# Optimization experiments

Measured on AMD Instinct MI355X. Metric: run time of the kernel, lower is better.

## Reference

```python
import jax, jax.numpy as jnp
import numpy as np

USER_NUM, ITEM_NUM = 50000, 25000
N_U, N_I = 4096, 4096
N_E, N_PRED = 262144, 65536
D, K, N_LAYERS = 64, 1000, 3
SSL_TEMP, SSL_REG, ALPHA, PROTO_REG = 0.1, 1e-6, 1.0, 8e-8


def setup_inputs() -> dict:
    key = jax.random.key(0)
    ks = jax.random.split(key, 16)
    return {
        "emb_user": jax.random.normal(ks[0], (USER_NUM, D), jnp.float32),
        "emb_item": jax.random.normal(ks[1], (ITEM_NUM, D), jnp.float32),
        "user_centroids": jax.random.normal(ks[2], (K, D), jnp.float32),
        "item_centroids": jax.random.normal(ks[3], (K, D), jnp.float32),
        "edge_u": jax.random.randint(ks[4], (N_E,), 0, N_U, jnp.int32),
        "edge_v": jax.random.randint(ks[5], (N_E,), 0, N_I, jnp.int32),
        "pos_u": jax.random.randint(ks[6], (N_PRED,), 0, N_U, jnp.int32),
        "pos_v": jax.random.randint(ks[7], (N_PRED,), 0, N_I, jnp.int32),
        "neg_u": jax.random.randint(ks[8], (N_PRED,), 0, N_U, jnp.int32),
        "neg_v": jax.random.randint(ks[9], (N_PRED,), 0, N_I, jnp.int32),
        "idx_user": jax.random.randint(ks[10], (N_U,), 0, USER_NUM, jnp.int32),
        "idx_item": jax.random.randint(ks[11], (N_I,), 0, ITEM_NUM, jnp.int32),
        "user2cluster": jax.random.randint(ks[12], (USER_NUM,), 0, K, jnp.int32),
        "item2cluster": jax.random.randint(ks[13], (ITEM_NUM,), 0, K, jnp.int32),
    }


def _l2norm(x, eps=1e-12):  # F.normalize(p=2, dim=1)
    return x / jnp.maximum(jnp.linalg.norm(x, axis=1, keepdims=True), eps)


def _ssl_loss(cur, prev, prev_total):
    nc, npv, nt = _l2norm(cur), _l2norm(prev), _l2norm(prev_total)
    pos = jnp.exp(jnp.sum(nc * npv, axis=1) / SSL_TEMP)            # [B]
    tot = jnp.exp(nc @ nt.T / SSL_TEMP).sum(axis=1)                 # [B]
    return -jnp.log(pos / tot).sum()


def _proto_loss(emb, idx, node2cluster, centroids):
    ne = _l2norm(emb)
    cents = _l2norm(centroids)                                      # run_kmeans normalizes centroids
    my_cent = cents[node2cluster[idx]]                              # [B, D]
    pos = jnp.exp(jnp.sum(ne * my_cent, axis=1) / SSL_TEMP)
    tot = jnp.exp(ne @ cents.T / SSL_TEMP).sum(axis=1)
    return -jnp.log(pos / tot).sum()


def reference(emb_user, emb_item, user_centroids, item_centroids,
              edge_u, edge_v, pos_u, pos_v, neg_u, neg_v,
              idx_user, idx_item, user2cluster, item2cluster):
    # --- symmetric-normalized bipartite GraphConv (norm='both', no weight/bias) ---
    ones_e = jnp.ones((N_E,), jnp.float32)
    deg_u = jax.ops.segment_sum(ones_e, edge_u, num_segments=N_U)
    deg_i = jax.ops.segment_sum(ones_e, edge_v, num_segments=N_I)
    inv_u = (1.0 / jnp.sqrt(jnp.maximum(deg_u, 1.0)))[:, None]      # [N_U,1]
    inv_i = (1.0 / jnp.sqrt(jnp.maximum(deg_i, 1.0)))[:, None]      # [N_I,1]

    e_u = emb_user[idx_user]                                        # initial subgraph embeddings
    e_i = emb_item[idx_item]
    res_u, res_i = e_u, e_i
    h_u, h_i = e_u, e_i
    for _ in range(N_LAYERS):
        m_u = (h_u * inv_u)[edge_u]                                 # messages along rate edges
        m_i = (h_i * inv_i)[edge_v]                                 # messages along rated-by edges
        new_i = jax.ops.segment_sum(m_u, edge_v, num_segments=N_I) * inv_i
        new_u = jax.ops.segment_sum(m_i, edge_u, num_segments=N_U) * inv_u
        h_u, h_i = new_u, new_i
        res_u = res_u + h_u
        res_i = res_i + h_i

    # --- structural-neighbour SSL loss (last layer output vs layer-0 embeddings) ---
    ssl_u = _ssl_loss(h_u, e_u, emb_user)
    ssl_i = _ssl_loss(h_i, e_i, emb_item)
    ssl_loss = SSL_REG * (ssl_u + ALPHA * ssl_i)

    # --- protoNCE loss (raw embedding-table rows vs kmeans centroids) ---
    proto_loss = PROTO_REG * (
        _proto_loss(emb_user[idx_user], idx_user, user2cluster, user_centroids)
        + _proto_loss(emb_item[idx_item], idx_item, item2cluster, item_centroids)
    )

    res_u = res_u / (N_LAYERS + 1)
    res_i = res_i / (N_LAYERS + 1)

    # --- HeteroDotProductPredictor: u_dot_v on 'rate' edges -> [E,1] ---
    pos_score = jnp.sum(res_u[pos_u] * res_i[pos_v], axis=1, keepdims=True)
    neg_score = jnp.sum(res_u[neg_u] * res_i[neg_v], axis=1, keepdims=True)
    return pos_score, neg_score, ssl_loss, proto_loss
```

## Files before the change

kernel.cpp:

```cpp
#include <hip/hip_runtime.h>
#include <hip/hip_bf16.h>

#define NU 4096
#define NI 4096
#define NE 262144
#define NPRED 65536
#define DD 64
#define KCL 1000
#define UNUM 50000
#define INUM 25000
#define INUM_PAD 25008
#define KCL_PAD 1008

typedef short sh8 __attribute__((ext_vector_type(8)));
typedef float f4 __attribute__((ext_vector_type(4)));

__device__ __forceinline__ float wred64(float x){
#pragma unroll
  for(int m=1;m<64;m<<=1) x += __shfl_xor(x,m);
  return x;
}

__device__ __forceinline__ float fast_exp2(float x){
  return __builtin_amdgcn_exp2f(x);
}

#define HB 1024
#define HN0 (HB+12500)
#define HN1 (HN0+6252)
#define HN2 (HN1+252)
#define HN3 (HN2+252)

__global__ void k_histnorm(const int* __restrict__ eu, const int* __restrict__ ev,
                           int* cu, int* ci,
                           const float* __restrict__ emb_u, const float* __restrict__ emb_i,
                           const float* __restrict__ ucent, const float* __restrict__ icent,
                           __hip_bfloat16* ntb_u, __hip_bfloat16* ntb_i,
                           __hip_bfloat16* ncb_u, __hip_bfloat16* ncb_i){
  int b = blockIdx.x;
  if(b < HB){
    int t = b*256 + threadIdx.x;
    atomicAdd(&cu[eu[t]],1); atomicAdd(&ci[ev[t]],1);
    return;
  }
  const float* in; __hip_bfloat16* outp; int rows; int base;
  if(b < HN0)      { in=emb_u; outp=ntb_u; rows=UNUM; base=HB; }
  else if(b < HN1) { in=emb_i; outp=ntb_i; rows=INUM; base=HN0; }
  else if(b < HN2) { in=ucent; outp=ncb_u; rows=KCL;  base=HN1; }
  else             { in=icent; outp=ncb_i; rows=KCL;  base=HN2; }
  int row = (b-base)*4 + (threadIdx.x>>6);
  int lane = threadIdx.x & 63;
  if(row >= rows){ outp[row*DD + lane] = __float2bfloat16(0.f); return; }
  float v = in[row*DD + lane];
  float s = wred64(v*v);
  float sc = 1.0f / fmaxf(sqrtf(s), 1e-12f);
  outp[row*DD + lane] = __float2bfloat16(v*sc);
}

__global__ void k_scan(const int* cnt_u, int* rp_u, int* cur_u, float* inv_u,
                       const int* cnt_i, int* rp_i, int* cur_i, float* inv_i,
                       float* tot4){
  {
    int base = blockIdx.x*8192 + threadIdx.x*8;
#pragma unroll
    for(int k=0;k<8;k++) tot4[base+k] = 0.f;
  }
  const int* cnt = blockIdx.x ? cnt_i : cnt_u;
  int* rp  = blockIdx.x ? rp_i  : rp_u;
  int* cur = blockIdx.x ? cur_i : cur_u;
  float* inv = blockIdx.x ? inv_i : inv_u;
  __shared__ int sdata[1024];
  int tid = threadIdx.x;
  int v[4]; int s = 0;
#pragma unroll
  for(int k=0;k<4;k++){ v[k]=cnt[tid*4+k]; s+=v[k]; }
  sdata[tid]=s; __syncthreads();
  for(int off=1; off<1024; off<<=1){
    int add = (tid>=off)? sdata[tid-off] : 0;
    __syncthreads();
    if(tid>=off) sdata[tid] += add;
    __syncthreads();
  }
  int run = sdata[tid]-s;
#pragma unroll
  for(int k=0;k<4;k++){
    int idx = tid*4+k;
    rp[idx]=run; cur[idx]=run;
    inv[idx] = 1.0f/sqrtf(fmaxf((float)v[k],1.0f));
    run += v[k];
  }
  if(tid==1023) rp[4096]=run;
}

__global__ void k_fillgather(const int* __restrict__ eu, const int* __restrict__ ev,
                             int* cur_u, int* cur_i, int* adj_u, int* adj_i,
                             const float* __restrict__ emb_u, const float* __restrict__ emb_i,
                             const int* __restrict__ idx_u, const int* __restrict__ idx_i,
                             const float* __restrict__ inv_u, const float* __restrict__ inv_i,
                             float* e_u, float* e_i, float* res_u, float* res_i,
                             float* hs_u, float* hs_i){
  int b = blockIdx.x;
  if(b < 1024){
    int t = b*256 + threadIdx.x;
    int u=eu[t], v=ev[t];
    adj_u[atomicAdd(&cur_u[u],1)] = v;
    adj_i[atomicAdd(&cur_i[v],1)] = u;
  } else {
    int t = (b-1024)*256 + threadIdx.x;
    const int half = NU*DD;
    if(t < half){
      int r=t>>6;
      float v = emb_u[idx_u[r]*DD + (t&63)];
      e_u[t]=v; res_u[t]=v; hs_u[t]=v*inv_u[r];
    } else {
      int s=t-half; int r=s>>6;
      float v = emb_i[idx_i[r]*DD + (s&63)];
      e_i[s]=v; res_i[s]=v; hs_i[s]=v*inv_i[r];
    }
  }
}

__global__ void k_conv(const int* __restrict__ rp_i, const int* __restrict__ adj_i,
                       const float* __restrict__ hsu_in, const float* __restrict__ inv_i,
                       float* h_i, float* res_i, float* hsi_out,
                       const int* __restrict__ rp_u, const int* __restrict__ adj_u,
                       const float* __restrict__ hsi_in, const float* __restrict__ inv_u,
                       float* h_u, float* res_u, float* hsu_out){
  int b = blockIdx.x*4 + (threadIdx.x>>6);
  int lane = threadIdx.x & 63;
  const int* rp; const int* adj; const float* srcv; const float* inv;
  float *h, *res, *hso; int node;
  if(b < NI){ rp=rp_i; adj=adj_i; srcv=hsu_in; inv=inv_i; h=h_i; res=res_i; hso=hsi_out; node=b; }
  else      { node=b-NI; rp=rp_u; adj=adj_u; srcv=hsi_in; inv=inv_u; h=h_u; res=res_u; hso=hsu_out; }
  int s=rp[node], e=rp[node+1];
  float acc=0.f;
  for(int base=s; base<e; base+=64){
    int m = e-base;
    int myidx = adj[base + min(lane, m-1)];
    int kk = min(64, m);
    int k=0;
    for(; k+8<=kk; k+=8){
      int i0=__shfl(myidx,k  ), i1=__shfl(myidx,k+1),
          i2=__shfl(myidx,k+2), i3=__shfl(myidx,k+3),
          i4=__shfl(myidx,k+4), i5=__shfl(myidx,k+5),
          i6=__shfl(myidx,k+6), i7=__shfl(myidx,k+7);
      float v0=srcv[i0*DD+lane], v1=srcv[i1*DD+lane],
            v2=srcv[i2*DD+lane], v3=srcv[i3*DD+lane],
            v4=srcv[i4*DD+lane], v5=srcv[i5*DD+lane],
            v6=srcv[i6*DD+lane], v7=srcv[i7*DD+lane];
      acc += ((v0+v1)+(v2+v3)) + ((v4+v5)+(v6+v7));
    }
    for(; k<kk; k++) acc += srcv[__shfl(myidx,k)*DD+lane];
  }
  float iv = inv[node];
  float outv = acc*iv;
  h[node*DD+lane] = outv;
  res[node*DD+lane] += outv;
  hso[node*DD+lane] = outv*iv;
}

#define PB0 1024
#define PB1 (PB0+1024)
#define PB2 (PB1+1024)
#define PB3 (PB2+1024)
#define PB4 (PB3+1024)

__global__ void k_normpos(const float* __restrict__ h_u, const float* __restrict__ h_i,
                          const float* __restrict__ e_u, const float* __restrict__ e_i,
                          const float* __restrict__ ucent, const float* __restrict__ icent,
                          __hip_bfloat16* nc_u, __hip_bfloat16* nc_i,
                          __hip_bfloat16* npv_u, __hip_bfloat16* npv_i,
                          const int* __restrict__ idx_u, const int* __restrict__ idx_i,
                          const int* __restrict__ u2c, const int* __restrict__ i2c,
                          float* pos4){
  const float SC = 14.426950408889634f;
  int b = blockIdx.x;
  int lane = threadIdx.x & 63;
  if(b >= PB3){
    int w = (b-PB3)*4 + (threadIdx.x>>6);
    float hu=h_u[w*DD+lane], eu=e_u[w*DD+lane];
    float hi=h_i[w*DD+lane], ei=e_i[w*DD+lane];
    int cu = u2c[idx_u[w]], ci = i2c[idx_i[w]];
    float cuv = ucent[cu*DD+lane], civ = icent[ci*DD+lane];
    float hh = wred64(hu*hu), ee = wred64(eu*eu), he = wred64(hu*eu);
    float h2 = wred64(hi*hi), e2 = wred64(ei*ei), hei= wred64(hi*ei);
    float ccu= wred64(cuv*cuv), ecu = wred64(eu*cuv);
    float cci= wred64(civ*civ), eci = wred64(ei*civ);
    if(lane==0){
      const float eps=1e-12f;
      pos4[0*NU+w] = he  / (fmaxf(sqrtf(hh),eps)*fmaxf(sqrtf(ee),eps));
      pos4[1*NU+w] = hei / (fmaxf(sqrtf(h2),eps)*fmaxf(sqrtf(e2),eps));
      pos4[2*NU+w] = ecu / (fmaxf(sqrtf(ee),eps)*fmaxf(sqrtf(ccu),eps));
      pos4[3*NU+w] = eci / (fmaxf(sqrtf(e2),eps)*fmaxf(sqrtf(cci),eps));
    }
    return;
  }
  const float* in; __hip_bfloat16* outp; int base;
  if(b < PB0)      { in=h_u; outp=nc_u;  base=0; }
  else if(b < PB1) { in=h_i; outp=nc_i;  base=PB0; }
  else if(b < PB2) { in=e_u; outp=npv_u; base=PB1; }
  else             { in=e_i; outp=npv_i; base=PB2; }
  int row = (b-base)*4 + (threadIdx.x>>6);
  float v = in[row*DD + lane];
  float s = wred64(v*v);
  float sc = SC / fmaxf(sqrtf(s), 1e-12f);
  outp[row*DD + lane] = __float2bfloat16(v*sc);
}

struct EArg {
  const __hip_bfloat16* A; const __hip_bfloat16* B; float* tot;
  int nBpad; int jchunk; int ny;
};
struct SArg {
  const float* res_u; const float* res_i;
  const int* pu; const int* pv; const int* nu; const int* nv; float* out;
};
#define EGX 784

__global__ __launch_bounds__(256,4)
void k_expsum(EArg e0, EArg e1, EArg e2, EArg e3, SArg sc){
  if(blockIdx.z == 4){
    const int stride = EGX*256;
    const int limit = 2*NPRED*16;
    for(int t = blockIdx.x*256 + threadIdx.x; t < limit; t += stride){
      int pair = t >> 4;
      int sl = t & 15;
      int a,b;
      if(pair < NPRED){ a=sc.pu[pair]; b=sc.pv[pair]; }
      else { a=sc.nu[pair-NPRED]; b=sc.nv[pair-NPRED]; }
      f4 xu = *(const f4*)(sc.res_u + a*DD + sl*4);
      f4 xv = *(const f4*)(sc.res_i + b*DD + sl*4);
      float x = xu[0]*xv[0] + xu[1]*xv[1] + xu[2]*xv[2] + xu[3]*xv[3];
      x += __shfl_xor(x,1); x += __shfl_xor(x,2);
      x += __shfl_xor(x,4); x += __shfl_xor(x,8);
      if(sl==0) sc.out[pair] = x*(1.0f/16.0f);
    }
    return;
  }
  EArg e = (blockIdx.z==0)? e0 : (blockIdx.z==1)? e1 : (blockIdx.z==2)? e2 : e3;
  int bid = blockIdx.x;
  int g = bid >> 6, r6 = bid & 63;
  int y = 8*g + (r6 & 7);
  int x = r6 >> 3;
  if(y >= e.ny) return;
  int wave = threadIdx.x >> 6;
  int lane = threadIdx.x & 63;
  int row0 = (x*4 + wave)*128;
  int j_begin = y*e.jchunk;
  int j_end = min(j_begin + e.jchunk, e.nBpad);
  int r = lane & 15, kq = (lane>>4)*8;

  sh8 a0[8], a1[8];
#pragma unroll
  for(int t=0;t<8;t++){
    const short* ap = (const short*)(e.A + (row0 + t*16 + r)*DD);
    a0[t] = *(const sh8*)(ap + kq);
    a1[t] = *(const sh8*)(ap + kq + 32);
  }
  float acc[8][4];
#pragma unroll
  for(int t=0;t<8;t++)
#pragma unroll
    for(int q=0;q<4;q++) acc[t][q]=0.f;

  const short* bbase = (const short*)e.B;
  const short* bp0 = bbase + (j_begin + r)*DD + kq;
  sh8 b0 = *(const sh8*)(bp0);
  sh8 b1 = *(const sh8*)(bp0 + 32);

#pragma unroll 2
  for(int j0=j_begin; j0<j_end; j0+=16){
    const short* np = bbase + (j0 + 16 + r)*DD + kq;
    sh8 n0 = *(const sh8*)(np);
    sh8 n1 = *(const sh8*)(np + 32);
#pragma unroll
    for(int t=0;t<8;t++){
      f4 c = {0.f,0.f,0.f,0.f};
      c = __builtin_amdgcn_mfma_f32_16x16x32_bf16(a0[t], b0, c, 0,0,0);
      c = __builtin_amdgcn_mfma_f32_16x16x32_bf16(a1[t], b1, c, 0,0,0);
#pragma unroll
      for(int q=0;q<4;q++) acc[t][q] += fast_exp2(c[q]);
    }
    b0 = n0; b1 = n1;
  }
#pragma unroll
  for(int t=0;t<8;t++){
#pragma unroll
    for(int q=0;q<4;q++){
      float v = acc[t][q];
      v += __shfl_xor(v,1); v += __shfl_xor(v,2);
      v += __shfl_xor(v,4); v += __shfl_xor(v,8);
      if(r==0) atomicAdd(&e.tot[row0 + t*16 + (lane>>4)*4 + q], v);
    }
  }
}

__global__ void k_loss(const float* __restrict__ tot4, const float* __restrict__ pos4,
                       float* out){
  const float PI_ = (float)(INUM_PAD-INUM);
  const float PK_ = (float)(KCL_PAD-KCL);
  float s0=0,s1=0,s2=0,s3=0;
  for(int b=threadIdx.x; b<NU; b+=256){
    s0 += logf(tot4[0*NU+b])       - 10.f*pos4[0*NU+b];
    s1 += logf(tot4[1*NU+b] - PI_) - 10.f*pos4[1*NU+b];
    s2 += logf(tot4[2*NU+b] - PK_) - 10.f*pos4[2*NU+b];
    s3 += logf(tot4[3*NU+b] - PK_) - 10.f*pos4[3*NU+b];
  }
  s0=wred64(s0); s1=wred64(s1); s2=wred64(s2); s3=wred64(s3);
  __shared__ float ls[4][4];
  int lane=threadIdx.x&63, w=threadIdx.x>>6;
  if(lane==0){ ls[w][0]=s0; ls[w][1]=s1; ls[w][2]=s2; ls[w][3]=s3; }
  __syncthreads();
  if(threadIdx.x==0){
    float a=0,b2=0,c=0,d=0;
#pragma unroll
    for(int k=0;k<4;k++){ a+=ls[k][0]; b2+=ls[k][1]; c+=ls[k][2]; d+=ls[k][3]; }
    out[2*NPRED]   = 1e-6f*(a+b2);
    out[2*NPRED+1] = 8e-8f*(c+d);
  }
}

extern "C" void kernel_launch(void* const* d_in, const int* in_sizes, int n_in,
                              void* d_out, int out_size, void* d_ws, size_t ws_size,
                              hipStream_t stream) {
  const float* emb_user = (const float*)d_in[0];
  const float* emb_item = (const float*)d_in[1];
  const float* ucent    = (const float*)d_in[2];
  const float* icent    = (const float*)d_in[3];
  const int* edge_u = (const int*)d_in[4];
  const int* edge_v = (const int*)d_in[5];
  const int* pos_u  = (const int*)d_in[6];
  const int* pos_v  = (const int*)d_in[7];
  const int* neg_u  = (const int*)d_in[8];
  const int* neg_v  = (const int*)d_in[9];
  const int* idx_u  = (const int*)d_in[10];
  const int* idx_i  = (const int*)d_in[11];
  const int* u2c    = (const int*)d_in[12];
  const int* i2c    = (const int*)d_in[13];
  float* out = (float*)d_out;

  char* w = (char*)d_ws;
  auto alloc = [&](size_t bytes)->void*{
    void* p = (void*)w;
    w += (bytes + 255) & ~(size_t)255;
    return p;
  };
  int* cnt_u = (int*)alloc(NU*4);
  int* cnt_i = (int*)alloc(NI*4);
  int* rp_u  = (int*)alloc((NU+1)*4);
  int* rp_i  = (int*)alloc((NI+1)*4);
  int* cur_u = (int*)alloc(NU*4);
  int* cur_i = (int*)alloc(NI*4);
  int* adj_u = (int*)alloc((size_t)NE*4);
  int* adj_i = (int*)alloc((size_t)NE*4);
  float* inv_u = (float*)alloc(NU*4);
  float* inv_i = (float*)alloc(NI*4);
  float* e_u  = (float*)alloc((size_t)NU*DD*4);
  float* e_i  = (float*)alloc((size_t)NI*DD*4);
  float* h_u  = (float*)alloc((size_t)NU*DD*4);
  float* h_i  = (float*)alloc((size_t)NI*DD*4);
  float* hsA_u = (float*)alloc((size_t)NU*DD*4);
  float* hsA_i = (float*)alloc((size_t)NI*DD*4);
  float* hsB_u = (float*)alloc((size_t)NU*DD*4);
  float* hsB_i = (float*)alloc((size_t)NI*DD*4);
  float* res_u= (float*)alloc((size_t)NU*DD*4);
  float* res_i= (float*)alloc((size_t)NI*DD*4);
  __hip_bfloat16* ntb_user = (__hip_bfloat16*)alloc((size_t)(UNUM+48)*DD*2);
  __hip_bfloat16* ntb_item = (__hip_bfloat16*)alloc((size_t)(INUM_PAD+48)*DD*2);
  __hip_bfloat16* ncb_u = (__hip_bfloat16*)alloc((size_t)(KCL_PAD+48)*DD*2);
  __hip_bfloat16* ncb_i = (__hip_bfloat16*)alloc((size_t)(KCL_PAD+48)*DD*2);
  __hip_bfloat16* nc_u  = (__hip_bfloat16*)alloc((size_t)NU*DD*2);
  __hip_bfloat16* nc_i  = (__hip_bfloat16*)alloc((size_t)NI*DD*2);
  __hip_bfloat16* npv_u = (__hip_bfloat16*)alloc((size_t)NU*DD*2);
  __hip_bfloat16* npv_i = (__hip_bfloat16*)alloc((size_t)NI*DD*2);
  float* tot4 = (float*)alloc(4*NU*4);
  float* pos4 = (float*)alloc(4*NU*4);

  hipMemsetAsync(cnt_u, 0, 2*NU*4, stream);

  k_histnorm<<<HN3, 256, 0, stream>>>(edge_u, edge_v, cnt_u, cnt_i,
                                      emb_user, emb_item, ucent, icent,
                                      ntb_user, ntb_item, ncb_u, ncb_i);
  k_scan<<<2, 1024, 0, stream>>>(cnt_u, rp_u, cur_u, inv_u,
                                 cnt_i, rp_i, cur_i, inv_i, tot4);
  k_fillgather<<<3072, 256, 0, stream>>>(edge_u, edge_v, cur_u, cur_i, adj_u, adj_i,
                                         emb_user, emb_item, idx_u, idx_i,
                                         inv_u, inv_i,
                                         e_u, e_i, res_u, res_i, hsA_u, hsA_i);
  k_conv<<<(NU+NI)/4, 256, 0, stream>>>(rp_i, adj_i, hsA_u, inv_i, h_i, res_i, hsB_i,
                                        rp_u, adj_u, hsA_i, inv_u, h_u, res_u, hsB_u);
  k_conv<<<(NU+NI)/4, 256, 0, stream>>>(rp_i, adj_i, hsB_u, inv_i, h_i, res_i, hsA_i,
                                        rp_u, adj_u, hsB_i, inv_u, h_u, res_u, hsA_u);
  k_conv<<<(NU+NI)/4, 256, 0, stream>>>(rp_i, adj_i, hsA_u, inv_i, h_i, res_i, hsB_i,
                                        rp_u, adj_u, hsA_i, inv_u, h_u, res_u, hsB_u);

  k_normpos<<<PB4, 256, 0, stream>>>(h_u, h_i, e_u, e_i, ucent, icent,
                                     nc_u, nc_i, npv_u, npv_i,
                                     idx_u, idx_i, u2c, i2c, pos4);

  EArg eu_ = { nc_u,  ntb_user, tot4 + 0*NU, UNUM,     512, 98 };
  EArg ei_ = { nc_i,  ntb_item, tot4 + 1*NU, INUM_PAD, 512, 49 };
  EArg ep0 = { npv_u, ncb_u,    tot4 + 2*NU, KCL_PAD,  48,  21 };
  EArg ep1 = { npv_i, ncb_i,    tot4 + 3*NU, KCL_PAD,  48,  21 };
  SArg sc  = { res_u, res_i, pos_u, pos_v, neg_u, neg_v, out };
  k_expsum<<<dim3(EGX,1,5), 256, 0, stream>>>(eu_, ei_, ep0, ep1, sc);

  k_loss<<<1, 256, 0, stream>>>(tot4, pos4, out);
}
```

Measured before the change: 217.4 us.

## Fuse normalization into last conv and loss into expsum via last-block counter

Moves the normalize/bf16 conversion and positive-score computation into the last graph-convolution pass, so a separate k_normpos launch no longer re-reads h and e. It also flattens the 5×784 z-grid of k_expsum into a compact 1D grid that drops the wasted early-exit blocks, and folds the final loss reduction into k_expsum using an atomic completion counter. The counter is zeroed by the existing memset. The result is two fewer kernel launches and fewer idle blocks, at the cost of a serialized tail reduction in one block and extra branching in k_conv.

```diff
diff --git a/kernel.cpp b/kernel.cpp
--- a/kernel.cpp
+++ b/kernel.cpp
@@ -125,13 +125,29 @@
                        float* h_i, float* res_i, float* hsi_out,
                        const int* __restrict__ rp_u, const int* __restrict__ adj_u,
                        const float* __restrict__ hsi_in, const float* __restrict__ inv_u,
-                       float* h_u, float* res_u, float* hsu_out){
+                       float* h_u, float* res_u, float* hsu_out,
+                       const float* __restrict__ e_u, const float* __restrict__ e_i,
+                       const float* __restrict__ ucent, const float* __restrict__ icent,
+                       const int* __restrict__ idx_u, const int* __restrict__ idx_i,
+                       const int* __restrict__ u2c, const int* __restrict__ i2c,
+                       __hip_bfloat16* nc_u, __hip_bfloat16* nc_i,
+                       __hip_bfloat16* npv_u, __hip_bfloat16* npv_i,
+                       float* pos4, int last){
   int b = blockIdx.x*4 + (threadIdx.x>>6);
   int lane = threadIdx.x & 63;
   const int* rp; const int* adj; const float* srcv; const float* inv;
   float *h, *res, *hso; int node;
-  if(b < NI){ rp=rp_i; adj=adj_i; srcv=hsu_in; inv=inv_i; h=h_i; res=res_i; hso=hsi_out; node=b; }
-  else      { node=b-NI; rp=rp_u; adj=adj_u; srcv=hsi_in; inv=inv_u; h=h_u; res=res_u; hso=hsu_out; }
+  const float* eX; const float* cent; const int* idxX; const int* n2c;
+  __hip_bfloat16 *nc, *npv; float *posA, *posB;
+  if(b < NI){
+    rp=rp_i; adj=adj_i; srcv=hsu_in; inv=inv_i; h=h_i; res=res_i; hso=hsi_out; node=b;
+    eX=e_i; cent=icent; idxX=idx_i; n2c=i2c; nc=nc_i; npv=npv_i;
+    posA=pos4+1*NU; posB=pos4+3*NU;
+  } else {
+    node=b-NI; rp=rp_u; adj=adj_u; srcv=hsi_in; inv=inv_u; h=h_u; res=res_u; hso=hsu_out;
+    eX=e_u; cent=ucent; idxX=idx_u; n2c=u2c; nc=nc_u; npv=npv_u;
+    posA=pos4+0*NU; posB=pos4+2*NU;
+  }
   int s=rp[node], e=rp[node+1];
   float acc=0.f;
   for(int base=s; base<e; base+=64){
@@ -156,167 +172,163 @@
   float outv = acc*iv;
   h[node*DD+lane] = outv;
   res[node*DD+lane] += outv;
-  hso[node*DD+lane] = outv*iv;
-}
-
-#define PB0 1024
-#define PB1 (PB0+1024)
-#define PB2 (PB1+1024)
-#define PB3 (PB2+1024)
-#define PB4 (PB3+1024)
-
-__global__ void k_normpos(const float* __restrict__ h_u, const float* __restrict__ h_i,
-                          const float* __restrict__ e_u, const float* __restrict__ e_i,
-                          const float* __restrict__ ucent, const float* __restrict__ icent,
-                          __hip_bfloat16* nc_u, __hip_bfloat16* nc_i,
-                          __hip_bfloat16* npv_u, __hip_bfloat16* npv_i,
-                          const int* __restrict__ idx_u, const int* __restrict__ idx_i,
-                          const int* __restrict__ u2c, const int* __restrict__ i2c,
-                          float* pos4){
+  if(!last){
+    hso[node*DD+lane] = outv*iv;
+    return;
+  }
   const float SC = 14.426950408889634f;
-  int b = blockIdx.x;
-  int lane = threadIdx.x & 63;
-  if(b >= PB3){
-    int w = (b-PB3)*4 + (threadIdx.x>>6);
-    float hu=h_u[w*DD+lane], eu=e_u[w*DD+lane];
-    float hi=h_i[w*DD+lane], ei=e_i[w*DD+lane];
-    int cu = u2c[idx_u[w]], ci = i2c[idx_i[w]];
-    float cuv = ucent[cu*DD+lane], civ = icent[ci*DD+lane];
-    float hh = wred64(hu*hu), ee = wred64(eu*eu), he = wred64(hu*eu);
-    float h2 = wred64(hi*hi), e2 = wred64(ei*ei), hei= wred64(hi*ei);
-    float ccu= wred64(cuv*cuv), ecu = wred64(eu*cuv);
-    float cci= wred64(civ*civ), eci = wred64(ei*civ);
-    if(lane==0){
-      const float eps=1e-12f;
-      pos4[0*NU+w] = he  / (fmaxf(sqrtf(hh),eps)*fmaxf(sqrtf(ee),eps));
-      pos4[1*NU+w] = hei / (fmaxf(sqrtf(h2),eps)*fmaxf(sqrtf(e2),eps));
-      pos4[2*NU+w] = ecu / (fmaxf(sqrtf(ee),eps)*fmaxf(sqrtf(ccu),eps));
-      pos4[3*NU+w] = eci / (fmaxf(sqrtf(e2),eps)*fmaxf(sqrtf(cci),eps));
-    }
-    return;
-  }
-  const float* in; __hip_bfloat16* outp; int base;
-  if(b < PB0)      { in=h_u; outp=nc_u;  base=0; }
-  else if(b < PB1) { in=h_i; outp=nc_i;  base=PB0; }
-  else if(b < PB2) { in=e_u; outp=npv_u; base=PB1; }
-  else             { in=e_i; outp=npv_i; base=PB2; }
-  int row = (b-base)*4 + (threadIdx.x>>6);
-  float v = in[row*DD + lane];
-  float s = wred64(v*v);
-  float sc = SC / fmaxf(sqrtf(s), 1e-12f);
-  outp[row*DD + lane] = __float2bfloat16(v*sc);
+  const float eps = 1e-12f;
+  float ev = eX[node*DD+lane];
+  float hn = wred64(outv*outv);
+  float en = wred64(ev*ev);
+  float ihn = 1.0f/fmaxf(sqrtf(hn), eps);
+  float ien = 1.0f/fmaxf(sqrtf(en), eps);
+  nc [node*DD+lane] = __float2bfloat16(outv*(SC*ihn));
+  npv[node*DD+lane] = __float2bfloat16(ev  *(SC*ien));
+  int c = n2c[idxX[node]];
+  float cv = cent[c*DD+lane];
+  float he = wred64(outv*ev);
+  float cc = wred64(cv*cv);
+  float ec = wred64(ev*cv);
+  if(lane==0){
+    float icn = 1.0f/fmaxf(sqrtf(cc), eps);
+    posA[node] = he*ihn*ien;
+    posB[node] = ec*ien*icn;
+  }
 }
 
 struct EArg {
   const __hip_bfloat16* A; const __hip_bfloat16* B; float* tot;
   int nBpad; int jchunk; int ny;
 };
-struct SArg {
+struct LArg {
   const float* res_u; const float* res_i;
-  const int* pu; const int* pv; const int* nu; const int* nv; float* out;
+  const int* pu; const int* pv; const int* nu; const int* nv;
+  float* out; float* tot4; const float* pos4; unsigned* ctr;
 };
-#define EGX 784
+#define EB0 784
+#define EB1 (EB0+392)
+#define EB2 (EB1+168)
+#define EB3 (EB2+168)
+#define EBT (EB3+784)
 
 __global__ __launch_bounds__(256,4)
-void k_expsum(EArg e0, EArg e1, EArg e2, EArg e3, SArg sc){
-  if(blockIdx.z == 4){
-    const int stride = EGX*256;
+void k_expsum(EArg e0, EArg e1, EArg e2, EArg e3, LArg lc){
+  int bid = blockIdx.x;
+  int tid = threadIdx.x;
+  if(bid >= EB3){
+    const int stride = (EBT-EB3)*256;
     const int limit = 2*NPRED*16;
-    for(int t = blockIdx.x*256 + threadIdx.x; t < limit; t += stride){
+    for(int t = (bid-EB3)*256 + tid; t < limit; t += stride){
       int pair = t >> 4;
       int sl = t & 15;
       int a,b;
-      if(pair < NPRED){ a=sc.pu[pair]; b=sc.pv[pair]; }
-      else { a=sc.nu[pair-NPRED]; b=sc.nv[pair-NPRED]; }
-      f4 xu = *(const f4*)(sc.res_u + a*DD + sl*4);
-      f4 xv = *(const f4*)(sc.res_i + b*DD + sl*4);
+      if(pair < NPRED){ a=lc.pu[pair]; b=lc.pv[pair]; }
+      else { a=lc.nu[pair-NPRED]; b=lc.nv[pair-NPRED]; }
+      f4 xu = *(const f4*)(lc.res_u + a*DD + sl*4);
+      f4 xv = *(const f4*)(lc.res_i + b*DD + sl*4);
       float x = xu[0]*xv[0] + xu[1]*xv[1] + xu[2]*xv[2] + xu[3]*xv[3];
       x += __shfl_xor(x,1); x += __shfl_xor(x,2);
       x += __shfl_xor(x,4); x += __shfl_xor(x,8);
-      if(sl==0) sc.out[pair] = x*(1.0f/16.0f);
-    }
-    return;
-  }
-  EArg e = (blockIdx.z==0)? e0 : (blockIdx.z==1)? e1 : (blockIdx.z==2)? e2 : e3;
-  int bid = blockIdx.x;
-  int g = bid >> 6, r6 = bid & 63;
-  int y = 8*g + (r6 & 7);
-  int x = r6 >> 3;
-  if(y >= e.ny) return;
-  int wave = threadIdx.x >> 6;
-  int lane = threadIdx.x & 63;
-  int row0 = (x*4 + wave)*128;
-  int j_begin = y*e.jchunk;
-  int j_end = min(j_begin + e.jchunk, e.nBpad);
-  int r = lane & 15, kq = (lane>>4)*8;
-
-  sh8 a0[8], a1[8];
-#pragma unroll
-  for(int t=0;t<8;t++){
-    const short* ap = (const short*)(e.A + (row0 + t*16 + r)*DD);
-    a0[t] = *(const sh8*)(ap + kq);
-    a1[t] = *(const sh8*)(ap + kq + 32);
-  }
-  float acc[8][4];
-#pragma unroll
-  for(int t=0;t<8;t++)
-#pragma unroll
-    for(int q=0;q<4;q++) acc[t][q]=0.f;
-
-  const short* bbase = (const short*)e.B;
-  const short* bp0 = bbase + (j_begin + r)*DD + kq;
-  sh8 b0 = *(const sh8*)(bp0);
-  sh8 b1 = *(const sh8*)(bp0 + 32);
+      if(sl==0) lc.out[pair] = x*(1.0f/16.0f);
+    }
+  } else {
+    EArg e; int local;
+    if(bid < EB0)      { e = e0; local = bid; }
+    else if(bid < EB1) { e = e1; local = bid-EB0; }
+    else if(bid < EB2) { e = e2; local = bid-EB1; }
+    else               { e = e3; local = bid-EB2; }
+    int g = local >> 6, r6 = local & 63;
+    int y = 8*g + (r6 & 7);
+    int x = r6 >> 3;
+    if(y < e.ny){
+      int wave = tid >> 6;
+      int lane = tid & 63;
+      int row0 = (x*4 + wave)*128;
+      int j_begin = y*e.jchunk;
+      int j_end = min(j_begin + e.jchunk, e.nBpad);
+      int r = lane & 15, kq = (lane>>4)*8;
+
+      sh8 a0[8], a1[8];
+#pragma unroll
+      for(int t=0;t<8;t++){
+        const short* ap = (const short*)(e.A + (row0 + t*16 + r)*DD);
+        a0[t] = *(const sh8*)(ap + kq);
+        a1[t] = *(const sh8*)(ap + kq + 32);
+      }
+      float acc[8][4];
+#pragma unroll
+      for(int t=0;t<8;t++)
+#pragma unroll
+        for(int q=0;q<4;q++) acc[t][q]=0.f;
+
+      const short* bbase = (const short*)e.B;
+      const short* bp0 = bbase + (j_begin + r)*DD + kq;
+      sh8 b0 = *(const sh8*)(bp0);
+      sh8 b1 = *(const sh8*)(bp0 + 32);
 
 #pragma unroll 2
-  for(int j0=j_begin; j0<j_end; j0+=16){
-    const short* np = bbase + (j0 + 16 + r)*DD + kq;
-    sh8 n0 = *(const sh8*)(np);
-    sh8 n1 = *(const sh8*)(np + 32);
-#pragma unroll
-    for(int t=0;t<8;t++){
-      f4 c = {0.f,0.f,0.f,0.f};
-      c = __builtin_amdgcn_mfma_f32_16x16x32_bf16(a0[t], b0, c, 0,0,0);
-      c = __builtin_amdgcn_mfma_f32_16x16x32_bf16(a1[t], b1, c, 0,0,0);
-#pragma unroll
-      for(int q=0;q<4;q++) acc[t][q] += fast_exp2(c[q]);
-    }
-    b0 = n0; b1 = n1;
-  }
-#pragma unroll
-  for(int t=0;t<8;t++){
-#pragma unroll
-    for(int q=0;q<4;q++){
-      float v = acc[t][q];
-      v += __shfl_xor(v,1); v += __shfl_xor(v,2);
-      v += __shfl_xor(v,4); v += __shfl_xor(v,8);
-      if(r==0) atomicAdd(&e.tot[row0 + t*16 + (lane>>4)*4 + q], v);
-    }
-  }
-}
-
-__global__ void k_loss(const float* __restrict__ tot4, const float* __restrict__ pos4,
-                       float* out){
-  const float PI_ = (float)(INUM_PAD-INUM);
-  const float PK_ = (float)(KCL_PAD-KCL);
-  float s0=0,s1=0,s2=0,s3=0;
-  for(int b=threadIdx.x; b<NU; b+=256){
-    s0 += logf(tot4[0*NU+b])       - 10.f*pos4[0*NU+b];
-    s1 += logf(tot4[1*NU+b] - PI_) - 10.f*pos4[1*NU+b];
-    s2 += logf(tot4[2*NU+b] - PK_) - 10.f*pos4[2*NU+b];
-    s3 += logf(tot4[3*NU+b] - PK_) - 10.f*pos4[3*NU+b];
-  }
-  s0=wred64(s0); s1=wred64(s1); s2=wred64(s2); s3=wred64(s3);
-  __shared__ float ls[4][4];
-  int lane=threadIdx.x&63, w=threadIdx.x>>6;
-  if(lane==0){ ls[w][0]=s0; ls[w][1]=s1; ls[w][2]=s2; ls[w][3]=s3; }
+      for(int j0=j_begin; j0<j_end; j0+=16){
+        const short* np = bbase + (j0 + 16 + r)*DD + kq;
+        sh8 n0 = *(const sh8*)(np);
+        sh8 n1 = *(const sh8*)(np + 32);
+#pragma unroll
+        for(int t=0;t<8;t++){
+          f4 c = {0.f,0.f,0.f,0.f};
+          c = __builtin_amdgcn_mfma_f32_16x16x32_bf16(a0[t], b0, c, 0,0,0);
+          c = __builtin_amdgcn_mfma_f32_16x16x32_bf16(a1[t], b1, c, 0,0,0);
+#pragma unroll
+          for(int q=0;q<4;q++) acc[t][q] += fast_exp2(c[q]);
+        }
+        b0 = n0; b1 = n1;
+      }
+#pragma unroll
+      for(int t=0;t<8;t++){
+#pragma unroll
+        for(int q=0;q<4;q++){
+          float v = acc[t][q];
+          v += __shfl_xor(v,1); v += __shfl_xor(v,2);
+          v += __shfl_xor(v,4); v += __shfl_xor(v,8);
+          if(r==0) atomicAdd(&e.tot[row0 + t*16 + (lane>>4)*4 + q], v);
+        }
+      }
+    }
+  }
+  __shared__ int s_done;
+  if(tid == 0){
+    __threadfence();
+    unsigned old = atomicAdd(lc.ctr, 1u);
+    s_done = (old == (unsigned)(EBT-1)) ? 1 : 0;
+  }
   __syncthreads();
-  if(threadIdx.x==0){
-    float a=0,b2=0,c=0,d=0;
-#pragma unroll
-    for(int k=0;k<4;k++){ a+=ls[k][0]; b2+=ls[k][1]; c+=ls[k][2]; d+=ls[k][3]; }
-    out[2*NPRED]   = 1e-6f*(a+b2);
-    out[2*NPRED+1] = 8e-8f*(c+d);
+  if(s_done){
+    const float PI_ = (float)(INUM_PAD-INUM);
+    const float PK_ = (float)(KCL_PAD-KCL);
+    float* tot4 = lc.tot4;
+    const float* pos4 = lc.pos4;
+    float s0=0,s1=0,s2=0,s3=0;
+    for(int b=tid; b<NU; b+=256){
+      float t0 = __hip_atomic_load(&tot4[0*NU+b], __ATOMIC_RELAXED, __HIP_MEMORY_SCOPE_AGENT);
+      float t1 = __hip_atomic_load(&tot4[1*NU+b], __ATOMIC_RELAXED, __HIP_MEMORY_SCOPE_AGENT);
+      float t2 = __hip_atomic_load(&tot4[2*NU+b], __ATOMIC_RELAXED, __HIP_MEMORY_SCOPE_AGENT);
+      float t3 = __hip_atomic_load(&tot4[3*NU+b], __ATOMIC_RELAXED, __HIP_MEMORY_SCOPE_AGENT);
+      s0 += logf(t0)       - 10.f*pos4[0*NU+b];
+      s1 += logf(t1 - PI_) - 10.f*pos4[1*NU+b];
+      s2 += logf(t2 - PK_) - 10.f*pos4[2*NU+b];
+      s3 += logf(t3 - PK_) - 10.f*pos4[3*NU+b];
+    }
+    s0=wred64(s0); s1=wred64(s1); s2=wred64(s2); s3=wred64(s3);
+    __shared__ float ls[4][4];
+    int lane=tid&63, w=tid>>6;
+    if(lane==0){ ls[w][0]=s0; ls[w][1]=s1; ls[w][2]=s2; ls[w][3]=s3; }
+    __syncthreads();
+    if(tid==0){
+      float a=0,b2=0,c=0,d=0;
+#pragma unroll
+      for(int k=0;k<4;k++){ a+=ls[k][0]; b2+=ls[k][1]; c+=ls[k][2]; d+=ls[k][3]; }
+      lc.out[2*NPRED]   = 1e-6f*(a+b2);
+      lc.out[2*NPRED+1] = 8e-8f*(c+d);
+    }
   }
 }
 
@@ -347,6 +359,7 @@
   };
   int* cnt_u = (int*)alloc(NU*4);
   int* cnt_i = (int*)alloc(NI*4);
+  unsigned* ctr = (unsigned*)alloc(256);
   int* rp_u  = (int*)alloc((NU+1)*4);
   int* rp_i  = (int*)alloc((NI+1)*4);
   int* cur_u = (int*)alloc(NU*4);
@@ -376,7 +389,7 @@
   float* tot4 = (float*)alloc(4*NU*4);
   float* pos4 = (float*)alloc(4*NU*4);
 
-  hipMemsetAsync(cnt_u, 0, 2*NU*4, stream);
+  hipMemsetAsync(cnt_u, 0, 2*NU*4 + 256, stream);
 
   k_histnorm<<<HN3, 256, 0, stream>>>(edge_u, edge_v, cnt_u, cnt_i,
                                       emb_user, emb_item, ucent, icent,
@@ -388,22 +401,22 @@
                                          inv_u, inv_i,
                                          e_u, e_i, res_u, res_i, hsA_u, hsA_i);
   k_conv<<<(NU+NI)/4, 256, 0, stream>>>(rp_i, adj_i, hsA_u, inv_i, h_i, res_i, hsB_i,
-                                        rp_u, adj_u, hsA_i, inv_u, h_u, res_u, hsB_u);
+                                        rp_u, adj_u, hsA_i, inv_u, h_u, res_u, hsB_u,
+                                        e_u, e_i, ucent, icent, idx_u, idx_i, u2c, i2c,
+                                        nc_u, nc_i, npv_u, npv_i, pos4, 0);
   k_conv<<<(NU+NI)/4, 256, 0, stream>>>(rp_i, adj_i, hsB_u, inv_i, h_i, res_i, hsA_i,
-                                        rp_u, adj_u, hsB_i, inv_u, h_u, res_u, hsA_u);
+                                        rp_u, adj_u, hsB_i, inv_u, h_u, res_u, hsA_u,
+                                        e_u, e_i, ucent, icent, idx_u, idx_i, u2c, i2c,
+                                        nc_u, nc_i, npv_u, npv_i, pos4, 0);
   k_conv<<<(NU+NI)/4, 256, 0, stream>>>(rp_i, adj_i, hsA_u, inv_i, h_i, res_i, hsB_i,
-                                        rp_u, adj_u, hsA_i, inv_u, h_u, res_u, hsB_u);
-
-  k_normpos<<<PB4, 256, 0, stream>>>(h_u, h_i, e_u, e_i, ucent, icent,
-                                     nc_u, nc_i, npv_u, npv_i,
-                                     idx_u, idx_i, u2c, i2c, pos4);
+                                        rp_u, adj_u, hsA_i, inv_u, h_u, res_u, hsB_u,
+                                        e_u, e_i, ucent, icent, idx_u, idx_i, u2c, i2c,
+                                        nc_u, nc_i, npv_u, npv_i, pos4, 1);
 
   EArg eu_ = { nc_u,  ntb_user, tot4 + 0*NU, UNUM,     512, 98 };
   EArg ei_ = { nc_i,  ntb_item, tot4 + 1*NU, INUM_PAD, 512, 49 };
   EArg ep0 = { npv_u, ncb_u,    tot4 + 2*NU, KCL_PAD,  48,  21 };
   EArg ep1 = { npv_i, ncb_i,    tot4 + 3*NU, KCL_PAD,  48,  21 };
-  SArg sc  = { res_u, res_i, pos_u, pos_v, neg_u, neg_v, out };
-  k_expsum<<<dim3(EGX,1,5), 256, 0, stream>>>(eu_, ei_, ep0, ep1, sc);
-
-  k_loss<<<1, 256, 0, stream>>>(tot4, pos4, out);
-}
+  LArg lc  = { res_u, res_i, pos_u, pos_v, neg_u, neg_v, out, tot4, pos4, ctr };
+  k_expsum<<<EBT, 256, 0, stream>>>(eu_, ei_, ep0, ep1, lc);
+}
```

Result: slower. 253.1 us (+16.4%).
